# Optimization experiments

Measured on AMD Instinct MI355X. Metric: run time of the kernel, lower is better.

Reference implementation:

```python
import jax, jax.numpy as jnp
import numpy as np

B, L, H, DK, DV = 4, 2048, 8, 64, 64


def setup_inputs() -> dict:
    key = jax.random.key(0)
    ks = jax.random.split(key, 5)
    s = 0.05
    return {
        "x": jax.random.normal(ks[0], (B, L, DV), dtype=jnp.float32),
        "wq": jax.random.normal(ks[1], (DV, H * DK), dtype=jnp.float32) * s,
        "bq": jnp.zeros((H * DK,), dtype=jnp.float32),
        "wk": jax.random.normal(ks[2], (DV, H * DK), dtype=jnp.float32) * s,
        "bk": jnp.zeros((H * DK,), dtype=jnp.float32),
        "wv": jax.random.normal(ks[3], (DV, H * DV), dtype=jnp.float32) * s,
        "bv": jnp.zeros((H * DV,), dtype=jnp.float32),
        "wo": jax.random.normal(ks[4], (H * DV, DV), dtype=jnp.float32) * s,
        "bo": jnp.zeros((DV,), dtype=jnp.float32),
    }


def reference(x, wq, bq, wk, bk, wv, bv, wo, bo):
    b, l, _ = x.shape
    # QKV projections -> [B, H, L, d]
    q = (x @ wq + bq).reshape(b, l, H, DK).transpose(0, 2, 1, 3)
    k = (x @ wk + bk).reshape(b, l, H, DK).transpose(0, 2, 1, 3)
    v = (x @ wv + bv).reshape(b, l, H, DV).transpose(0, 2, 1, 3)
    # NOTE: original MULTIPLIES by sqrt(dk) (a quirk), not divides.
    align = jnp.einsum('bhqd,bhkd->bhqk', q, k) * jnp.sqrt(jnp.float32(DK))
    align = jax.nn.softmax(align, axis=-1)
    # Equivalent to the tile/multiply/reduce_sum: sum_k align[...,k] * v[...,k,:]
    ctx = jnp.einsum('bhqk,bhkv->bhqv', align, v)  # [B, H, L, DV]
    # NOTE: original transposes to [B, L, DV, H] before flattening (dv-major).
    ctx = ctx.transpose(0, 2, 3, 1).reshape(b, l, DV * H)
    return ctx @ wo + bo
```

## Files before the change

kernel.cpp:

```cpp
#include <hip/hip_runtime.h>


typedef _Float16 half4v __attribute__((ext_vector_type(4)));
typedef _Float16 half8v __attribute__((ext_vector_type(8)));
typedef float    float4v __attribute__((ext_vector_type(4)));

#define BB   4
#define LL   2048
#define HH   8
#define DKV  64
#define NROW (BB * LL)
#define QSCALE 11.541560327111707f

#define KVBLK 64
#define NKB   (LL / KVBLK)

#define GLOAD_LDS(gp, sp) \
    __builtin_amdgcn_global_load_lds((const __attribute__((address_space(1))) void*)(gp), \
                                     (__attribute__((address_space(3))) void*)(sp), 16, 0, 0)

__global__ __launch_bounds__(256) void k_prep_x(const float* __restrict__ x,
                                                _Float16* __restrict__ xh) {
    int i = blockIdx.x * 256 + threadIdx.x;
    float4v v = ((const float4v*)x)[i];
    half4v h;
    h[0] = (_Float16)v[0]; h[1] = (_Float16)v[1];
    h[2] = (_Float16)v[2]; h[3] = (_Float16)v[3];
    ((half4v*)xh)[i] = h;
}

__global__ __launch_bounds__(256) void k_prep_w(const float* __restrict__ wq, const float* __restrict__ bq,
                                                const float* __restrict__ wk, const float* __restrict__ bk,
                                                const float* __restrict__ wv, const float* __restrict__ bv,
                                                _Float16* __restrict__ wt, float* __restrict__ biasc) {
    int idx = blockIdx.x * 256 + threadIdx.x;
    int j = idx >> 6, i = idx & 63;
    const float* w; const float* bsrc; int jj; float sc = 1.0f;
    if (j < 512)       { w = wq; bsrc = bq; jj = j;        sc = QSCALE; }
    else if (j < 1024) { w = wk; bsrc = bk; jj = j - 512;  }
    else               { w = wv; bsrc = bv; jj = j - 1024; }
    wt[idx] = (_Float16)(w[i * 512 + jj] * sc);
    if (i == 0) biasc[j] = bsrc[jj] * sc;
}

__global__ __launch_bounds__(256) void k_prep_wo(const float* __restrict__ wo,
                                                 _Float16* __restrict__ wo2t) {
    int idx = blockIdx.x * 256 + threadIdx.x;
    int j = idx >> 9, k = idx & 511;
    int dv = k & 63, h = k >> 6;
    wo2t[idx] = (_Float16)wo[(dv * HH + h) * 64 + j];
}

__global__ __launch_bounds__(256) void k_proj(const _Float16* __restrict__ xh,
                                              const _Float16* __restrict__ wt,
                                              const float* __restrict__ biasc,
                                              _Float16* __restrict__ qh,
                                              _Float16* __restrict__ kh,
                                              _Float16* __restrict__ vtw) {
    int wid = threadIdx.x >> 6, lane = threadIdx.x & 63;
    int g = lane >> 4, c = lane & 15;
    int m0 = blockIdx.x * 64 + wid * 16;
    int n0 = blockIdx.y * 64;

    half8v a0 = *(const half8v*)(xh + (m0 + c) * 64 + g * 8);
    half8v a1 = *(const half8v*)(xh + (m0 + c) * 64 + 32 + g * 8);

    float4v acc[4] = {};
#pragma unroll
    for (int t = 0; t < 4; ++t) {
        const _Float16* wp = wt + (n0 + t * 16 + c) * 64 + g * 8;
        half8v b0 = *(const half8v*)(wp);
        half8v b1 = *(const half8v*)(wp + 32);
        acc[t] = __builtin_amdgcn_mfma_f32_16x16x32_f16(a0, b0, acc[t], 0, 0, 0);
        acc[t] = __builtin_amdgcn_mfma_f32_16x16x32_f16(a1, b1, acc[t], 0, 0, 0);
    }
#pragma unroll
    for (int t = 0; t < 4; ++t) {
        int j = n0 + t * 16 + c;
        float bias = biasc[j];
        int mat = j >> 9, jj = j & 511, h = jj >> 6;
        if (mat == 2) {
            int b = m0 >> 11, l0 = m0 & 2047;
            half4v hv;
#pragma unroll
            for (int r = 0; r < 4; ++r) hv[r] = (_Float16)(acc[t][r] + bias);
            *(half4v*)(vtw + ((size_t)(b * 8 + h) * 64 + t * 16 + c) * 2048 + l0 + g * 4) = hv;
        } else {
            int cc = (t * 16 + c);
            _Float16* dst = (mat == 0) ? qh : kh;
#pragma unroll
            for (int r = 0; r < 4; ++r) {
                int m = m0 + g * 4 + r;
                int b = m >> 11, l = m & 2047;
                dst[((size_t)(b * HH + h) * LL + l) * 64 + cc] = (_Float16)(acc[t][r] + bias);
            }
        }
    }
}

__global__ __launch_bounds__(512) void k_attn(const _Float16* __restrict__ qh,
                                              const _Float16* __restrict__ kh,
                                              const _Float16* __restrict__ vt,
                                              _Float16* __restrict__ ctx) {
    __shared__ char lds[2 * 16384];

    int tid = threadIdx.x;
    int wid = tid >> 6, lane = tid & 63;
    int g = lane >> 4, c = lane & 15;

    int bid = blockIdx.x;
    int xcd = bid & 7;
    int rest = bid >> 3;
    int bh = xcd * 4 + (rest >> 4);
    int qc = rest & 15;
    int q0 = qc * 128 + wid * 16;

    const _Float16* qp = qh + ((size_t)bh * LL + q0) * 64;
    const char* kg = (const char*)(kh + (size_t)bh * LL * 64);
    const char* vg = (const char*)(vt + (size_t)bh * 64 * LL);

    half8v qf0 = *(const half8v*)(qp + c * 64 + g * 8);
    half8v qf1 = *(const half8v*)(qp + c * 64 + 32 + g * 8);

    int pK   = wid * 1024 + lane * 16;
    int rowS = pK >> 7;
    int srcK = (pK & ~127) | ((pK & 127) ^ ((rowS & 7) << 4));
    size_t srcV = (size_t)rowS * (LL * 2) + (size_t)((pK & 127) ^ ((rowS & 7) << 4));

#define STAGE(buf, kb) do {                                                   \
        char* sK = lds + (buf) * 16384 + wid * 1024;                          \
        char* sV = lds + (buf) * 16384 + 8192 + wid * 1024;                   \
        GLOAD_LDS(kg + (size_t)(kb) * 8192 + srcK, sK);                       \
        GLOAD_LDS(vg + srcV + (size_t)(kb) * 128, sV);                        \
    } while (0)

    float4v o[4] = {};
    float m = -1e30f, lsum = 0.0f;
    int swzk_c = (c & 7) << 4;

    STAGE(0, 0);

    for (int kb = 0; kb < NKB; ++kb) {
        int cur = kb & 1;
        if (kb + 1 < NKB) {
            STAGE(cur ^ 1, kb + 1);
            asm volatile("s_waitcnt vmcnt(2)" ::: "memory");
        } else {
            asm volatile("s_waitcnt vmcnt(0)" ::: "memory");
        }
        asm volatile("s_barrier" ::: "memory");

        const char* lk = lds + cur * 16384;
        const char* lv = lk + 8192;

#pragma unroll
        for (int s = 0; s < 4; ++s) {
            int krow = s * 16 + c;
            int swzk = (krow & 7) << 4;
            half8v kf0 = *(const half8v*)(lk + krow * 128 + ((g * 16) ^ swzk));
            half8v kf1 = *(const half8v*)(lk + krow * 128 + ((g * 16 + 64) ^ swzk));
            float4v sv = {};
            sv = __builtin_amdgcn_mfma_f32_16x16x32_f16(kf0, qf0, sv, 0, 0, 0);
            sv = __builtin_amdgcn_mfma_f32_16x16x32_f16(kf1, qf1, sv, 0, 0, 0);

            float pmax = fmaxf(fmaxf(sv[0], sv[1]), fmaxf(sv[2], sv[3]));
            pmax = fmaxf(pmax, __shfl_xor(pmax, 16));
            pmax = fmaxf(pmax, __shfl_xor(pmax, 32));

            if (__any(pmax > m + 3.0f)) {
                float mn = fmaxf(m, pmax);
                float sc = __builtin_amdgcn_exp2f(m - mn);
                lsum *= sc;
#pragma unroll
                for (int t = 0; t < 4; ++t) o[t] *= sc;
                m = mn;
            }

            float p0 = __builtin_amdgcn_exp2f(sv[0] - m);
            float p1 = __builtin_amdgcn_exp2f(sv[1] - m);
            float p2 = __builtin_amdgcn_exp2f(sv[2] - m);
            float p3 = __builtin_amdgcn_exp2f(sv[3] - m);
            lsum += (p0 + p1) + (p2 + p3);
            half4v ph;
            ph[0] = (_Float16)p0; ph[1] = (_Float16)p1;
            ph[2] = (_Float16)p2; ph[3] = (_Float16)p3;

            int vcol = (s * 32 + g * 8) ^ swzk_c;
#pragma unroll
            for (int t = 0; t < 4; ++t) {
                half4v vf = *(const half4v*)(lv + (t * 16 + c) * 128 + vcol);
                o[t] = __builtin_amdgcn_mfma_f32_16x16x16f16(vf, ph, o[t], 0, 0, 0);
            }
        }

        asm volatile("s_barrier" ::: "memory");
    }
#undef STAGE

    lsum += __shfl_xor(lsum, 16);
    lsum += __shfl_xor(lsum, 32);
    float inv = 1.0f / lsum;

    _Float16* cp = ctx + ((size_t)bh * LL + q0 + c) * 64 + g * 4;
#pragma unroll
    for (int t = 0; t < 4; ++t) {
        half4v hv;
#pragma unroll
        for (int r = 0; r < 4; ++r) hv[r] = (_Float16)(o[t][r] * inv);
        *(half4v*)(cp + t * 16) = hv;
    }
}

__global__ __launch_bounds__(64) void k_oproj(const _Float16* __restrict__ ctx,
                                              const _Float16* __restrict__ wo2t,
                                              const float* __restrict__ bo,
                                              float* __restrict__ out) {
    int lane = threadIdx.x & 63;
    int g = lane >> 4, c = lane & 15;
    int m0 = blockIdx.x * 16;
    int b = m0 >> 11, l = m0 & 2047;
    const _Float16* cbase = ctx + ((size_t)b * HH * LL + l) * 64;

    float4v acc[4] = {};
#pragma unroll
    for (int kc = 0; kc < 16; ++kc) {
        int hh = kc >> 1;
        const _Float16* ap = cbase + (size_t)hh * LL * 64 + c * 64 + (kc & 1) * 32 + g * 8;
        half8v a = *(const half8v*)(ap);
#pragma unroll
        for (int t = 0; t < 4; ++t) {
            half8v bf = *(const half8v*)(wo2t + (t * 16 + c) * 512 + kc * 32 + g * 8);
            acc[t] = __builtin_amdgcn_mfma_f32_16x16x32_f16(a, bf, acc[t], 0, 0, 0);
        }
    }
#pragma unroll
    for (int t = 0; t < 4; ++t) {
        float bias = bo[t * 16 + c];
#pragma unroll
        for (int r = 0; r < 4; ++r) {
            int mm = m0 + g * 4 + r;
            out[mm * 64 + t * 16 + c] = acc[t][r] + bias;
        }
    }
}

extern "C" void kernel_launch(void* const* d_in, const int* in_sizes, int n_in,
                              void* d_out, int out_size, void* d_ws, size_t ws_size,
                              hipStream_t stream) {
    const float* x  = (const float*)d_in[0];
    const float* wq = (const float*)d_in[1];
    const float* bq = (const float*)d_in[2];
    const float* wk = (const float*)d_in[3];
    const float* bk = (const float*)d_in[4];
    const float* wv = (const float*)d_in[5];
    const float* bv = (const float*)d_in[6];
    const float* wo = (const float*)d_in[7];
    const float* bo = (const float*)d_in[8];
    float* out = (float*)d_out;

    char* ws = (char*)d_ws;
    _Float16* xh    = (_Float16*)(ws);
    _Float16* wt    = (_Float16*)(ws + 1048576);
    float*    biasc = (float*)   (ws + 1245184);
    _Float16* wo2t  = (_Float16*)(ws + 1251328);
    _Float16* qh    = (_Float16*)(ws + 1316864);
    _Float16* kh    = (_Float16*)(ws + 1316864 + 1ull * 8388608);
    _Float16* vt    = (_Float16*)(ws + 1316864 + 2ull * 8388608);
    _Float16* ctx   = (_Float16*)(ws + 1316864 + 3ull * 8388608);

    hipLaunchKernelGGL(k_prep_x,  dim3(512),      dim3(256), 0, stream, x, xh);
    hipLaunchKernelGGL(k_prep_w,  dim3(384),      dim3(256), 0, stream, wq, bq, wk, bk, wv, bv, wt, biasc);
    hipLaunchKernelGGL(k_prep_wo, dim3(128),      dim3(256), 0, stream, wo, wo2t);
    hipLaunchKernelGGL(k_proj,    dim3(128, 24),  dim3(256), 0, stream, xh, wt, biasc, qh, kh, vt);
    hipLaunchKernelGGL(k_attn,    dim3(512),      dim3(512), 0, stream, qh, kh, vt, ctx);
    hipLaunchKernelGGL(k_oproj,   dim3(512),      dim3(64),  0, stream, ctx, wo2t, bo, out);
}
```

Measured before the change: 110.0 us.

## Process two 16-row query tiles per wave in attention to reuse K/V fragments

Each wave in the attention kernel now handles 32 query rows as two independent 16-row tiles with separate online-softmax state. K and V fragments read from LDS are shared by both tiles, and each block covers 256 queries, which halves the grid to 256 blocks and halves K/V global staging per query. This cuts LDS reads and global traffic per unit of work and interleaves two independent MFMA chains. In exchange it uses more registers and gives fewer blocks than the 256 CUs can spread across, which may lower occupancy.

```diff
diff --git a/kernel.cpp b/kernel.cpp
--- a/kernel.cpp
+++ b/kernel.cpp
@@ -111,16 +111,18 @@
     int bid = blockIdx.x;
     int xcd = bid & 7;
     int rest = bid >> 3;
-    int bh = xcd * 4 + (rest >> 4);
-    int qc = rest & 15;
-    int q0 = qc * 128 + wid * 16;
+    int bh = xcd * 4 + (rest >> 3);
+    int qc = rest & 7;
+    int q0 = qc * 256 + wid * 32;
 
     const _Float16* qp = qh + ((size_t)bh * LL + q0) * 64;
     const char* kg = (const char*)(kh + (size_t)bh * LL * 64);
     const char* vg = (const char*)(vt + (size_t)bh * 64 * LL);
 
-    half8v qf0 = *(const half8v*)(qp + c * 64 + g * 8);
-    half8v qf1 = *(const half8v*)(qp + c * 64 + 32 + g * 8);
+    half8v qa0 = *(const half8v*)(qp + c * 64 + g * 8);
+    half8v qa1 = *(const half8v*)(qp + c * 64 + 32 + g * 8);
+    half8v qb0 = *(const half8v*)(qp + (16 + c) * 64 + g * 8);
+    half8v qb1 = *(const half8v*)(qp + (16 + c) * 64 + 32 + g * 8);
 
     int pK   = wid * 1024 + lane * 16;
     int rowS = pK >> 7;
@@ -134,8 +136,9 @@
         GLOAD_LDS(vg + srcV + (size_t)(kb) * 128, sV);                        \
     } while (0)
 
-    float4v o[4] = {};
-    float m = -1e30f, lsum = 0.0f;
+    float4v oa[4] = {}, ob[4] = {};
+    float ma = -1e30f, lsumA = 0.0f;
+    float mb = -1e30f, lsumB = 0.0f;
     int swzk_c = (c & 7) << 4;
 
     STAGE(0, 0);
@@ -159,37 +162,60 @@
             int swzk = (krow & 7) << 4;
             half8v kf0 = *(const half8v*)(lk + krow * 128 + ((g * 16) ^ swzk));
             half8v kf1 = *(const half8v*)(lk + krow * 128 + ((g * 16 + 64) ^ swzk));
-            float4v sv = {};
-            sv = __builtin_amdgcn_mfma_f32_16x16x32_f16(kf0, qf0, sv, 0, 0, 0);
-            sv = __builtin_amdgcn_mfma_f32_16x16x32_f16(kf1, qf1, sv, 0, 0, 0);
-
-            float pmax = fmaxf(fmaxf(sv[0], sv[1]), fmaxf(sv[2], sv[3]));
-            pmax = fmaxf(pmax, __shfl_xor(pmax, 16));
-            pmax = fmaxf(pmax, __shfl_xor(pmax, 32));
-
-            if (__any(pmax > m + 3.0f)) {
-                float mn = fmaxf(m, pmax);
-                float sc = __builtin_amdgcn_exp2f(m - mn);
-                lsum *= sc;
-#pragma unroll
-                for (int t = 0; t < 4; ++t) o[t] *= sc;
-                m = mn;
+
+            float4v sva = {};
+            sva = __builtin_amdgcn_mfma_f32_16x16x32_f16(kf0, qa0, sva, 0, 0, 0);
+            sva = __builtin_amdgcn_mfma_f32_16x16x32_f16(kf1, qa1, sva, 0, 0, 0);
+            float4v svb = {};
+            svb = __builtin_amdgcn_mfma_f32_16x16x32_f16(kf0, qb0, svb, 0, 0, 0);
+            svb = __builtin_amdgcn_mfma_f32_16x16x32_f16(kf1, qb1, svb, 0, 0, 0);
+
+            float pmaxa = fmaxf(fmaxf(sva[0], sva[1]), fmaxf(sva[2], sva[3]));
+            pmaxa = fmaxf(pmaxa, __shfl_xor(pmaxa, 16));
+            pmaxa = fmaxf(pmaxa, __shfl_xor(pmaxa, 32));
+            if (__any(pmaxa > ma + 3.0f)) {
+                float mn = fmaxf(ma, pmaxa);
+                float sc = __builtin_amdgcn_exp2f(ma - mn);
+                lsumA *= sc;
+#pragma unroll
+                for (int t = 0; t < 4; ++t) oa[t] *= sc;
+                ma = mn;
             }
-
-            float p0 = __builtin_amdgcn_exp2f(sv[0] - m);
-            float p1 = __builtin_amdgcn_exp2f(sv[1] - m);
-            float p2 = __builtin_amdgcn_exp2f(sv[2] - m);
-            float p3 = __builtin_amdgcn_exp2f(sv[3] - m);
-            lsum += (p0 + p1) + (p2 + p3);
-            half4v ph;
-            ph[0] = (_Float16)p0; ph[1] = (_Float16)p1;
-            ph[2] = (_Float16)p2; ph[3] = (_Float16)p3;
+            float pa0 = __builtin_amdgcn_exp2f(sva[0] - ma);
+            float pa1 = __builtin_amdgcn_exp2f(sva[1] - ma);
+            float pa2 = __builtin_amdgcn_exp2f(sva[2] - ma);
+            float pa3 = __builtin_amdgcn_exp2f(sva[3] - ma);
+            lsumA += (pa0 + pa1) + (pa2 + pa3);
+            half4v pha;
+            pha[0] = (_Float16)pa0; pha[1] = (_Float16)pa1;
+            pha[2] = (_Float16)pa2; pha[3] = (_Float16)pa3;
+
+            float pmaxb = fmaxf(fmaxf(svb[0], svb[1]), fmaxf(svb[2], svb[3]));
+            pmaxb = fmaxf(pmaxb, __shfl_xor(pmaxb, 16));
+            pmaxb = fmaxf(pmaxb, __shfl_xor(pmaxb, 32));
+            if (__any(pmaxb > mb + 3.0f)) {
+                float mn = fmaxf(mb, pmaxb);
+                float sc = __builtin_amdgcn_exp2f(mb - mn);
+                lsumB *= sc;
+#pragma unroll
+                for (int t = 0; t < 4; ++t) ob[t] *= sc;
+                mb = mn;
+            }
+            float pb0 = __builtin_amdgcn_exp2f(svb[0] - mb);
+            float pb1 = __builtin_amdgcn_exp2f(svb[1] - mb);
+            float pb2 = __builtin_amdgcn_exp2f(svb[2] - mb);
+            float pb3 = __builtin_amdgcn_exp2f(svb[3] - mb);
+            lsumB += (pb0 + pb1) + (pb2 + pb3);
+            half4v phb;
+            phb[0] = (_Float16)pb0; phb[1] = (_Float16)pb1;
+            phb[2] = (_Float16)pb2; phb[3] = (_Float16)pb3;
 
             int vcol = (s * 32 + g * 8) ^ swzk_c;
 #pragma unroll
             for (int t = 0; t < 4; ++t) {
                 half4v vf = *(const half4v*)(lv + (t * 16 + c) * 128 + vcol);
-                o[t] = __builtin_amdgcn_mfma_f32_16x16x16f16(vf, ph, o[t], 0, 0, 0);
+                oa[t] = __builtin_amdgcn_mfma_f32_16x16x16f16(vf, pha, oa[t], 0, 0, 0);
+                ob[t] = __builtin_amdgcn_mfma_f32_16x16x16f16(vf, phb, ob[t], 0, 0, 0);
             }
         }
 
@@ -197,17 +223,25 @@
     }
 #undef STAGE
 
-    lsum += __shfl_xor(lsum, 16);
-    lsum += __shfl_xor(lsum, 32);
-    float inv = 1.0f / lsum;
-
-    _Float16* cp = ctx + ((size_t)bh * LL + q0 + c) * 64 + g * 4;
+    lsumA += __shfl_xor(lsumA, 16);
+    lsumA += __shfl_xor(lsumA, 32);
+    lsumB += __shfl_xor(lsumB, 16);
+    lsumB += __shfl_xor(lsumB, 32);
+    float inva = 1.0f / lsumA;
+    float invb = 1.0f / lsumB;
+
+    _Float16* cpa = ctx + ((size_t)bh * LL + q0 + c) * 64 + g * 4;
+    _Float16* cpb = cpa + 16 * 64;
 #pragma unroll
     for (int t = 0; t < 4; ++t) {
-        half4v hv;
-#pragma unroll
-        for (int r = 0; r < 4; ++r) hv[r] = (_Float16)(o[t][r] * inv);
-        *(half4v*)(cp + t * 16) = hv;
+        half4v hva, hvb;
+#pragma unroll
+        for (int r = 0; r < 4; ++r) {
+            hva[r] = (_Float16)(oa[t][r] * inva);
+            hvb[r] = (_Float16)(ob[t][r] * invb);
+        }
+        *(half4v*)(cpa + t * 16) = hva;
+        *(half4v*)(cpb + t * 16) = hvb;
     }
 }
 
@@ -272,6 +306,6 @@
     hipLaunchKernelGGL(k_prep_w,  dim3(384),      dim3(256), 0, stream, wq, bq, wk, bk, wv, bv, wt, biasc);
     hipLaunchKernelGGL(k_prep_wo, dim3(128),      dim3(256), 0, stream, wo, wo2t);
     hipLaunchKernelGGL(k_proj,    dim3(128, 24),  dim3(256), 0, stream, xh, wt, biasc, qh, kh, vt);
-    hipLaunchKernelGGL(k_attn,    dim3(512),      dim3(512), 0, stream, qh, kh, vt, ctx);
+    hipLaunchKernelGGL(k_attn,    dim3(256),      dim3(512), 0, stream, qh, kh, vt, ctx);
     hipLaunchKernelGGL(k_oproj,   dim3(512),      dim3(64),  0, stream, ctx, wo2t, bo, out);
 }
```

New measurement: 115.7 us. 5.2% more time.

## Split attention KV range across two wave halves and merge partial softmax states

Applied to the files above, without the earlier changes.

The attention kernel now processes 64 queries per block with two groups of four waves, each covering half of the KV sequence. The partial (m, lsum, o) states are merged through LDS at the end, flash-decoding style. The grid doubles to 1024 blocks for more parallelism, and double buffering is replaced by single-buffer stage/sync epochs with full waits. The row-max shuffles move inside the rescale branch. In exchange it adds an LDS merge step and fp16 rounding of the partial outputs, and the loss of load/compute overlap may stall on memory.

```diff
diff --git a/kernel.cpp b/kernel.cpp
--- a/kernel.cpp
+++ b/kernel.cpp
@@ -13,11 +13,16 @@
 #define QSCALE 11.541560327111707f
 
 #define KVBLK 64
-#define NKB   (LL / KVBLK)
+#define NEP   16
 
 #define GLOAD_LDS(gp, sp) \
     __builtin_amdgcn_global_load_lds((const __attribute__((address_space(1))) void*)(gp), \
                                      (__attribute__((address_space(3))) void*)(sp), 16, 0, 0)
+
+#define SYNC_FULL do {                                                        \
+        asm volatile("s_waitcnt vmcnt(0) lgkmcnt(0)" ::: "memory");           \
+        asm volatile("s_barrier" ::: "memory");                               \
+    } while (0)
 
 __global__ __launch_bounds__(256) void k_prep_x(const float* __restrict__ x,
                                                 _Float16* __restrict__ xh) {
@@ -98,22 +103,23 @@
     }
 }
 
-__global__ __launch_bounds__(512) void k_attn(const _Float16* __restrict__ qh,
-                                              const _Float16* __restrict__ kh,
-                                              const _Float16* __restrict__ vt,
-                                              _Float16* __restrict__ ctx) {
-    __shared__ char lds[2 * 16384];
+__global__ __launch_bounds__(512, 4) void k_attn(const _Float16* __restrict__ qh,
+                                                 const _Float16* __restrict__ kh,
+                                                 const _Float16* __restrict__ vt,
+                                                 _Float16* __restrict__ ctx) {
+    __shared__ char lds[32768];
 
     int tid = threadIdx.x;
     int wid = tid >> 6, lane = tid & 63;
     int g = lane >> 4, c = lane & 15;
+    int qw = wid & 3, half = wid >> 2;
 
     int bid = blockIdx.x;
     int xcd = bid & 7;
     int rest = bid >> 3;
-    int bh = xcd * 4 + (rest >> 4);
-    int qc = rest & 15;
-    int q0 = qc * 128 + wid * 16;
+    int bh = xcd * 4 + (rest >> 5);
+    int qc = rest & 31;
+    int q0 = qc * 64 + qw * 16;
 
     const _Float16* qp = qh + ((size_t)bh * LL + q0) * 64;
     const char* kg = (const char*)(kh + (size_t)bh * LL * 64);
@@ -122,36 +128,43 @@
     half8v qf0 = *(const half8v*)(qp + c * 64 + g * 8);
     half8v qf1 = *(const half8v*)(qp + c * 64 + 32 + g * 8);
 
-    int pK   = wid * 1024 + lane * 16;
-    int rowS = pK >> 7;
-    int srcK = (pK & ~127) | ((pK & 127) ^ ((rowS & 7) << 4));
-    size_t srcV = (size_t)rowS * (LL * 2) + (size_t)((pK & 127) ^ ((rowS & 7) << 4));
-
-#define STAGE(buf, kb) do {                                                   \
-        char* sK = lds + (buf) * 16384 + wid * 1024;                          \
-        char* sV = lds + (buf) * 16384 + 8192 + wid * 1024;                   \
-        GLOAD_LDS(kg + (size_t)(kb) * 8192 + srcK, sK);                       \
-        GLOAD_LDS(vg + srcV + (size_t)(kb) * 128, sV);                        \
+    int isV = (wid >> 1) & 1, hs = wid >> 2, sub = wid & 1;
+    const char* sbase[4];
+    int estride;
+    if (!isV) {
+        estride = KVBLK * 128;
+#pragma unroll
+        for (int j = 0; j < 4; ++j) {
+            int p = sub * 4096 + j * 1024 + lane * 16;
+            int row = p >> 7, col = p & 127;
+            sbase[j] = kg + (size_t)hs * 131072 + row * 128 + (col ^ ((row & 7) << 4));
+        }
+    } else {
+        estride = KVBLK * 2;
+#pragma unroll
+        for (int j = 0; j < 4; ++j) {
+            int p = sub * 4096 + j * 1024 + lane * 16;
+            int dv = p >> 7, kb = p & 127;
+            sbase[j] = vg + (size_t)dv * 4096 + hs * 2048 + (kb ^ ((dv & 7) << 4));
+        }
+    }
+
+#define STAGE(e) do {                                                         \
+        _Pragma("unroll") for (int j = 0; j < 4; ++j)                         \
+            GLOAD_LDS(sbase[j] + (size_t)(e) * estride, lds + wid * 4096 + j * 1024); \
     } while (0)
 
     float4v o[4] = {};
     float m = -1e30f, lsum = 0.0f;
     int swzk_c = (c & 7) << 4;
 
-    STAGE(0, 0);
-
-    for (int kb = 0; kb < NKB; ++kb) {
-        int cur = kb & 1;
-        if (kb + 1 < NKB) {
-            STAGE(cur ^ 1, kb + 1);
-            asm volatile("s_waitcnt vmcnt(2)" ::: "memory");
-        } else {
-            asm volatile("s_waitcnt vmcnt(0)" ::: "memory");
-        }
-        asm volatile("s_barrier" ::: "memory");
-
-        const char* lk = lds + cur * 16384;
-        const char* lv = lk + 8192;
+    STAGE(0);
+
+    const char* lk = lds + half * 16384;
+    const char* lv = lk + 8192;
+
+    for (int e = 0; e < NEP; ++e) {
+        SYNC_FULL;
 
 #pragma unroll
         for (int s = 0; s < 4; ++s) {
@@ -164,10 +177,9 @@
             sv = __builtin_amdgcn_mfma_f32_16x16x32_f16(kf1, qf1, sv, 0, 0, 0);
 
             float pmax = fmaxf(fmaxf(sv[0], sv[1]), fmaxf(sv[2], sv[3]));
-            pmax = fmaxf(pmax, __shfl_xor(pmax, 16));
-            pmax = fmaxf(pmax, __shfl_xor(pmax, 32));
-
             if (__any(pmax > m + 3.0f)) {
+                pmax = fmaxf(pmax, __shfl_xor(pmax, 16));
+                pmax = fmaxf(pmax, __shfl_xor(pmax, 32));
                 float mn = fmaxf(m, pmax);
                 float sc = __builtin_amdgcn_exp2f(m - mn);
                 lsum *= sc;
@@ -193,21 +205,55 @@
             }
         }
 
-        asm volatile("s_barrier" ::: "memory");
+        if (e + 1 < NEP) {
+            SYNC_FULL;
+            STAGE(e + 1);
+        }
     }
 #undef STAGE
 
-    lsum += __shfl_xor(lsum, 16);
-    lsum += __shfl_xor(lsum, 32);
-    float inv = 1.0f / lsum;
-
-    _Float16* cp = ctx + ((size_t)bh * LL + q0 + c) * 64 + g * 4;
-#pragma unroll
-    for (int t = 0; t < 4; ++t) {
-        half4v hv;
-#pragma unroll
-        for (int r = 0; r < 4; ++r) hv[r] = (_Float16)(o[t][r] * inv);
-        *(half4v*)(cp + t * 16) = hv;
+    SYNC_FULL;
+    if (half == 1) {
+        char* mr = lds + (qw * 64 + lane) * 48;
+#pragma unroll
+        for (int t = 0; t < 4; ++t) {
+            half4v hv;
+#pragma unroll
+            for (int r = 0; r < 4; ++r) hv[r] = (_Float16)o[t][r];
+            *(half4v*)(mr + t * 8) = hv;
+        }
+        *(float*)(mr + 32) = m;
+        *(float*)(mr + 36) = lsum;
+    }
+    SYNC_FULL;
+    if (half == 0) {
+        const char* mr = lds + (qw * 64 + lane) * 48;
+        float m2 = *(const float*)(mr + 32);
+        float l2 = *(const float*)(mr + 36);
+        float mN = fmaxf(m, m2);
+        float s1 = __builtin_amdgcn_exp2f(m - mN);
+        float s2 = __builtin_amdgcn_exp2f(m2 - mN);
+#pragma unroll
+        for (int t = 0; t < 4; ++t) {
+            half4v h2 = *(const half4v*)(mr + t * 8);
+#pragma unroll
+            for (int r = 0; r < 4; ++r)
+                o[t][r] = o[t][r] * s1 + (float)h2[r] * s2;
+        }
+        lsum = lsum * s1 + l2 * s2;
+
+        lsum += __shfl_xor(lsum, 16);
+        lsum += __shfl_xor(lsum, 32);
+        float inv = 1.0f / lsum;
+
+        _Float16* cp = ctx + ((size_t)bh * LL + q0 + c) * 64 + g * 4;
+#pragma unroll
+        for (int t = 0; t < 4; ++t) {
+            half4v hv;
+#pragma unroll
+            for (int r = 0; r < 4; ++r) hv[r] = (_Float16)(o[t][r] * inv);
+            *(half4v*)(cp + t * 16) = hv;
+        }
     }
 }
 
@@ -272,6 +318,6 @@
     hipLaunchKernelGGL(k_prep_w,  dim3(384),      dim3(256), 0, stream, wq, bq, wk, bk, wv, bv, wt, biasc);
     hipLaunchKernelGGL(k_prep_wo, dim3(128),      dim3(256), 0, stream, wo, wo2t);
     hipLaunchKernelGGL(k_proj,    dim3(128, 24),  dim3(256), 0, stream, xh, wt, biasc, qh, kh, vt);
-    hipLaunchKernelGGL(k_attn,    dim3(512),      dim3(512), 0, stream, qh, kh, vt, ctx);
+    hipLaunchKernelGGL(k_attn,    dim3(1024),     dim3(512), 0, stream, qh, kh, vt, ctx);
     hipLaunchKernelGGL(k_oproj,   dim3(512),      dim3(64),  0, stream, ctx, wo2t, bo, out);
 }
```

Result: no change. 110.7 us (+0.6%).
